# Kernel tuning notes

Measured on AMD Instinct MI355X. Metric: run time of the kernel, lower is better.

## Reference

```python
import jax, jax.numpy as jnp
import numpy as np
from jax import lax

silu = jax.nn.silu

def conv2d(x, w, b, pad):
    y = lax.conv_general_dilated(x, w, (1, 1), [(pad, pad), (pad, pad)],
                                 dimension_numbers=('NCHW', 'OIHW', 'NCHW'))
    return y + b[None, :, None, None]

def avgpool2(x):
    B, C, H, W = x.shape
    return x.reshape(B, C, H // 2, 2, W // 2, 2).mean(axis=(3, 5))

def up2x(x):
    # bilinear scale_factor=2, align_corners=True (matches F.interpolate)
    B, C, H, W = x.shape
    Ho, Wo = 2 * H, 2 * W
    ys = jnp.arange(Ho, dtype=x.dtype) * ((H - 1) / (Ho - 1))
    xs = jnp.arange(Wo, dtype=x.dtype) * ((W - 1) / (Wo - 1))
    y0 = jnp.floor(ys).astype(jnp.int32); y1 = jnp.minimum(y0 + 1, H - 1); wy = ys - y0
    x0 = jnp.floor(xs).astype(jnp.int32); x1 = jnp.minimum(x0 + 1, W - 1); wx = xs - x0
    row = x[:, :, y0, :] * (1 - wy)[None, None, :, None] + x[:, :, y1, :] * wy[None, None, :, None]
    return row[:, :, :, x0] * (1 - wx) + row[:, :, :, x1] * wx

def deform_conv2d(x, offset, weight, groups):
    # torchvision DeformConv2d semantics: stride=1, pad=(k-1)//2, dilation=1, no bias
    B, Cin, H, W = x.shape
    Cout, cpg, kh, kw = weight.shape  # cpg = Cin // groups
    K = kh * kw
    OG = offset.shape[1] // (2 * K)   # offset groups
    Cog = Cin // OG
    off = offset.reshape(B, OG, K, 2, H, W)  # (dy, dx) per kernel tap
    ki = jnp.repeat(jnp.arange(kh, dtype=x.dtype) - (kh - 1) // 2, kw)  # [K]
    kj = jnp.tile(jnp.arange(kw, dtype=x.dtype) - (kw - 1) // 2, kh)
    py = off[:, :, :, 0] + jnp.arange(H, dtype=x.dtype)[None, None, None, :, None] + ki[None, None, :, None, None]
    px = off[:, :, :, 1] + jnp.arange(W, dtype=x.dtype)[None, None, None, None, :] + kj[None, None, :, None, None]
    y0f = jnp.floor(py); x0f = jnp.floor(px)
    ly = py - y0f; lx = px - x0f
    y0 = y0f.astype(jnp.int32); x0 = x0f.astype(jnp.int32)
    xg = x.reshape(B, OG, Cog, H * W)

    def corner(yi, xi, wt):
        valid = (yi >= 0) & (yi < H) & (xi >= 0) & (xi < W)
        idx = jnp.clip(yi, 0, H - 1) * W + jnp.clip(xi, 0, W - 1)        # [B,OG,K,H,W]
        idxf = jnp.broadcast_to(idx.reshape(B, OG, 1, K * H * W), (B, OG, Cog, K * H * W))
        v = jnp.take_along_axis(xg, idxf, axis=3).reshape(B, OG, Cog, K, H, W)
        return v * (wt * valid)[:, :, None]

    val = (corner(y0, x0, (1 - ly) * (1 - lx)) + corner(y0, x0 + 1, (1 - ly) * lx)
           + corner(y0 + 1, x0, ly * (1 - lx)) + corner(y0 + 1, x0 + 1, ly * lx))
    # grouped contraction over sampled taps
    valg = val.reshape(B, groups, Cin // groups, K, H, W)
    wg = weight.reshape(groups, Cout // groups, cpg, K)
    return jnp.einsum('bgckhw,gock->bgohw', valg, wg).reshape(B, Cout, H, W)

def setup_inputs() -> dict:
    key = jax.random.key(0)
    ks = iter(jax.random.split(key, 64))
    def w(shape, s=0.05):
        return jax.random.normal(next(ks), shape, jnp.float32) * s
    B, H, W = 4, 512, 512
    d = {'x': jax.random.normal(next(ks), (B, 4, H, W), jnp.float32)}
    # offset estimators (small scale so sampled offsets stay moderate)
    d['eo1_w1'] = w((18, 4, 5, 5), 0.02);  d['eo1_b1'] = w((18,), 0.02)
    d['eo1_w2'] = w((36, 18, 5, 5), 0.02); d['eo1_b2'] = w((36,), 0.02)
    d['dcw1'] = w((2, 2, 3, 3))            # DeformConv2d(4->2, groups=2)
    d['c1d_w1'] = w((4, 2, 3, 3));   d['c1d_b1'] = w((4,))
    d['c1d_w2'] = w((8, 4, 3, 3));   d['c1d_b2'] = w((8,))
    d['eo2_w1'] = w((18, 8, 5, 5), 0.02);  d['eo2_b1'] = w((18,), 0.02)
    d['eo2_w2'] = w((36, 18, 5, 5), 0.02); d['eo2_b2'] = w((36,), 0.02)
    d['dcw2'] = w((8, 4, 3, 3))            # DeformConv2d(8->8, groups=2)
    d['c2d_w1'] = w((12, 8, 3, 3));  d['c2d_b1'] = w((12,))
    d['c2d_w2'] = w((16, 12, 3, 3)); d['c2d_b2'] = w((16,))
    d['eo3_w1'] = w((18, 16, 5, 5), 0.02); d['eo3_b1'] = w((18,), 0.02)
    d['eo3_w2'] = w((36, 18, 5, 5), 0.02); d['eo3_b2'] = w((36,), 0.02)
    d['dcw3'] = w((16, 8, 3, 3))           # DeformConv2d(16->16, groups=2)
    d['c3d_w1'] = w((14, 16, 3, 3)); d['c3d_b1'] = w((14,))
    d['c3d_w2'] = w((12, 14, 3, 3)); d['c3d_b2'] = w((12,))
    d['up2_w'] = w((12, 12, 3, 3));  d['up2_b'] = w((12,))
    d['c2u_w1'] = w((16, 28, 3, 3)); d['c2u_b1'] = w((16,))
    d['c2u_w2'] = w((8, 16, 3, 3));  d['c2u_b2'] = w((8,))
    d['up1_w'] = w((8, 8, 3, 3));    d['up1_b'] = w((8,))
    d['c1u_w1'] = w((8, 16, 3, 3));  d['c1u_b1'] = w((8,))
    d['c1u_w2'] = w((2, 8, 3, 3));   d['c1u_b2'] = w((2,))
    return d

def reference(x, eo1_w1, eo1_b1, eo1_w2, eo1_b2, dcw1, c1d_w1, c1d_b1, c1d_w2, c1d_b2,
              eo2_w1, eo2_b1, eo2_w2, eo2_b2, dcw2, c2d_w1, c2d_b1, c2d_w2, c2d_b2,
              eo3_w1, eo3_b1, eo3_w2, eo3_b2, dcw3, c3d_w1, c3d_b1, c3d_w2, c3d_b2,
              up2_w, up2_b, c2u_w1, c2u_b1, c2u_w2, c2u_b2, up1_w, up1_b,
              c1u_w1, c1u_b1, c1u_w2, c1u_b2):
    def convbasic(h, w1, b1, w2, b2):
        return silu(conv2d(silu(conv2d(h, w1, b1, 1)), w2, b2, 1))
    # level 1 down
    off1 = conv2d(conv2d(x, eo1_w1, eo1_b1, 2), eo1_w2, eo1_b2, 2)
    comp1 = deform_conv2d(x, off1, dcw1, groups=2)
    conv1_d = convbasic(comp1, c1d_w1, c1d_b1, c1d_w2, c1d_b2)
    pool1 = avgpool2(conv1_d)
    # level 2 down
    off2 = conv2d(conv2d(pool1, eo2_w1, eo2_b1, 2), eo2_w2, eo2_b2, 2)
    comp2 = deform_conv2d(pool1, off2, dcw2, groups=2)
    conv2_d = convbasic(comp2, c2d_w1, c2d_b1, c2d_w2, c2d_b2)
    pool2 = avgpool2(conv2_d)
    # level 3 (bottleneck)
    off3 = conv2d(conv2d(pool2, eo3_w1, eo3_b1, 2), eo3_w2, eo3_b2, 2)
    comp3 = deform_conv2d(pool2, off3, dcw3, groups=2)
    conv3_d = convbasic(comp3, c3d_w1, c3d_b1, c3d_w2, c3d_b2)
    # up path
    usmpl2 = silu(conv2d(up2x(conv3_d), up2_w, up2_b, 1))
    conv2_u = convbasic(jnp.concatenate([usmpl2, conv2_d], axis=1), c2u_w1, c2u_b1, c2u_w2, c2u_b2)
    usmpl1 = silu(conv2d(up2x(conv2_u), up1_w, up1_b, 1))
    conv1_u = convbasic(jnp.concatenate([usmpl1, conv1_d], axis=1), c1u_w1, c1u_b1, c1u_w2, c1u_b2)
    return conv1_u
```

## Files before the change

kernel.cpp:

```cpp
#include <hip/hip_runtime.h>
#include <math.h>

#define THREADS 256
typedef __attribute__((ext_vector_type(2))) float f32x2;
typedef __attribute__((ext_vector_type(4))) float f32x4;

__device__ __forceinline__ float silu_f(float v) {
    return v / (1.f + __expf(-v));
}

__device__ __forceinline__ void pk_fma_lo(f32x2& d, f32x2 a, f32x2 b) {
    asm("v_pk_fma_f32 %0, %1, %2, %0 op_sel:[0,0,0] op_sel_hi:[0,1,1]"
        : "+v"(d) : "v"(a), "v"(b));
}
__device__ __forceinline__ void pk_fma_hi(f32x2& d, f32x2 a, f32x2 b) {
    asm("v_pk_fma_f32 %0, %1, %2, %0 op_sel:[1,0,0] op_sel_hi:[1,1,1]"
        : "+v"(d) : "v"(a), "v"(b));
}
__device__ __forceinline__ void pk_fma_lo_s(f32x2& d, f32x2 a, f32x2 b) {
    asm("v_pk_fma_f32 %0, %1, %2, %0 op_sel:[0,0,0] op_sel_hi:[0,1,1]"
        : "+v"(d) : "v"(a), "s"(b));
}
__device__ __forceinline__ void pk_fma_hi_s(f32x2& d, f32x2 a, f32x2 b) {
    asm("v_pk_fma_f32 %0, %1, %2, %0 op_sel:[1,0,0] op_sel_hi:[1,1,1]"
        : "+v"(d) : "v"(a), "s"(b));
}

struct TEnt { const float* src; int dst; int cin; int cout; int k2; int base; int n; };
struct TTab { TEnt e[40]; int total; };

__global__ __launch_bounds__(THREADS)
void transpose_w_k(TTab t, float* __restrict__ tw) {
    const int i = blockIdx.x * THREADS + threadIdx.x;
    if (i >= t.total) return;
    int j = 0;
    while (i >= t.e[j].base + t.e[j].n) ++j;
    const TEnt e = t.e[j];
    const int local = i - e.base;
    const int co  = local % e.cout;
    const int tmp = local / e.cout;
    const int k   = tmp % e.k2;
    const int ci  = tmp / e.k2;
    tw[e.dst + local] = e.src[(co * e.cin + ci) * e.k2 + k];
}

template<int KS, int PX>
__device__ __forceinline__ void load_row(float* __restrict__ rr,
                                         const float* __restrict__ rp,
                                         bool vy, int x0, int W)
{
    constexpr int PAD = (KS - 1) / 2;
    constexpr int RW = PX + KS - 1;
#pragma unroll
    for (int q = -1; q <= PX / 4; ++q) {
        if (4 * q + 3 + PAD < 0 || 4 * q + PAD >= RW) continue;
        const int xs = x0 + 4 * q;
        const bool safe = (q >= 0) && (4 * q + 3 < PX);
        float vc[4] = {0.f, 0.f, 0.f, 0.f};
        if (safe) {
            if (vy) {
                const float4 v = *reinterpret_cast<const float4*>(rp + xs);
                vc[0] = v.x; vc[1] = v.y; vc[2] = v.z; vc[3] = v.w;
            }
        } else if (vy && xs >= 0 && xs + 4 <= W) {
            const float4 v = *reinterpret_cast<const float4*>(rp + xs);
            vc[0] = v.x; vc[1] = v.y; vc[2] = v.z; vc[3] = v.w;
        } else if (vy) {
#pragma unroll
            for (int c = 0; c < 4; ++c)
                vc[c] = ((unsigned)(xs + c) < (unsigned)W) ? rp[xs + c] : 0.f;
        }
#pragma unroll
        for (int c = 0; c < 4; ++c) {
            const int t = 4 * q + c + PAD;
            if (t >= 0 && t < RW) rr[t] = vc[c];
        }
    }
}

template<int CIN, int COUT, int KS, int PX, int PHASE, int RW2, int NP>
__device__ __forceinline__ void chan_body(
    const float* __restrict__ ip0, const float* __restrict__ wz,
    int cl, int y, int x0, int W, int H, int lw, int total,
    f32x2 (&r2)[2][RW2], f32x2 (&wb)[2][NP], f32x2 (&acc)[NP][PX])
{
    constexpr int PAD = (KS - 1) / 2;
    constexpr int K2 = KS * KS;
    static_assert(K2 % 2 == 1, "parity continuity needs odd K2");
#pragma unroll
    for (int ky = 0; ky < KS; ++ky) {
        {
            const bool last = (ky + 1 == KS);
            const int ncl = cl + (last ? 1 : 0);
            const int nky = last ? 0 : (ky + 1);
            if (!last || ncl < CIN) {
                const int yy = y + nky - PAD;
                load_row<KS, PX>((float*)r2[(PHASE + ky + 1) & 1],
                                 ip0 + (size_t)ncl * total + (yy << lw),
                                 (unsigned)yy < (unsigned)H, x0, W);
            }
        }
#pragma unroll
        for (int kx = 0; kx < KS; ++kx) {
            const int t = ky * KS + kx;
            const int wc = (PHASE + t) & 1;
            if (t + 1 < K2 || cl + 1 < CIN) {
                const f32x2* __restrict__ nx =
                    (const f32x2*)(wz + (size_t)(cl * K2 + t + 1) * COUT);
#pragma unroll
                for (int p = 0; p < NP; ++p) wb[wc ^ 1][p] = nx[p];
            }
#pragma unroll
            for (int p = 0; p < NP; ++p) {
                const f32x2 wp = wb[wc][p];
#pragma unroll
                for (int j = 0; j < PX; ++j) {
                    const int e = kx + j;
                    if (e & 1) pk_fma_hi_s(acc[p][j], r2[(PHASE + ky) & 1][e >> 1], wp);
                    else       pk_fma_lo_s(acc[p][j], r2[(PHASE + ky) & 1][e >> 1], wp);
                }
            }
            __builtin_amdgcn_sched_barrier(0);
        }
    }
}

template<int CIN, int COUT, int KS, bool ACT, int PX>
__global__ __launch_bounds__(THREADS)
void conv_sl_k(const float* __restrict__ in, const float* __restrict__ wt,
               const float* __restrict__ bias, float* __restrict__ out,
               int H, int lw, int bs_in, int bs_out, int nb, int nz)
{
    constexpr int PAD = (KS - 1) / 2;
    constexpr int K2 = KS * KS;
    constexpr int NP = COUT / 2;
    constexpr int RW = PX + KS - 1;
    constexpr int RW2 = (RW + 1) / 2;
    static_assert(CIN % 2 == 0 && COUT % 2 == 0 && PX % 4 == 0, "");

    const int lin = blockIdx.x;
    const int r8 = lin & 7;
    int q = lin >> 3;
    const int z = q % nz; q /= nz;
    const int g = q * 8 + r8;
    const int b = g % nb;
    const int xb = g / nb;

    const float* __restrict__ wz = wt + (size_t)z * (CIN * K2 * COUT);
    const int W = 1 << lw;
    const int total = H << lw;
    const int idx = (xb * THREADS + threadIdx.x) * PX;
    const float* ip0 = in + (size_t)b * bs_in;
    float* op = out + (size_t)b * bs_out + (size_t)z * COUT * total;
    const int x0 = idx & (W - 1);
    const int y  = idx >> lw;

    f32x2 acc[NP][PX];
#pragma unroll
    for (int p = 0; p < NP; ++p) {
        f32x2 bb;
        bb.x = bias[z * COUT + 2 * p];
        bb.y = bias[z * COUT + 2 * p + 1];
#pragma unroll
        for (int j = 0; j < PX; ++j) acc[p][j] = bb;
    }

    f32x2 r2[2][RW2];
    f32x2 wb[2][NP];
    {
        const int yy = y - PAD;
        load_row<KS, PX>((float*)r2[0], ip0 + (yy << lw),
                         (unsigned)yy < (unsigned)H, x0, W);
        const f32x2* __restrict__ w0 = (const f32x2*)wz;
#pragma unroll
        for (int p = 0; p < NP; ++p) wb[0][p] = w0[p];
    }

#pragma unroll 1
    for (int c2 = 0; c2 < CIN / 2; ++c2) {
        chan_body<CIN, COUT, KS, PX, 0, RW2, NP>(ip0, wz, 2 * c2,     y, x0, W, H, lw, total, r2, wb, acc);
        chan_body<CIN, COUT, KS, PX, 1, RW2, NP>(ip0, wz, 2 * c2 + 1, y, x0, W, H, lw, total, r2, wb, acc);
    }

#pragma unroll
    for (int p = 0; p < NP; ++p) {
#pragma unroll
        for (int h = 0; h < 2; ++h) {
            const int co = 2 * p + h;
#pragma unroll
            for (int j4 = 0; j4 < PX / 4; ++j4) {
                float4 v;
                float a0 = h ? acc[p][4 * j4 + 0].y : acc[p][4 * j4 + 0].x;
                float a1 = h ? acc[p][4 * j4 + 1].y : acc[p][4 * j4 + 1].x;
                float a2 = h ? acc[p][4 * j4 + 2].y : acc[p][4 * j4 + 2].x;
                float a3 = h ? acc[p][4 * j4 + 3].y : acc[p][4 * j4 + 3].x;
                v.x = ACT ? silu_f(a0) : a0;
                v.y = ACT ? silu_f(a1) : a1;
                v.z = ACT ? silu_f(a2) : a2;
                v.w = ACT ? silu_f(a3) : a3;
                *reinterpret_cast<float4*>(op + (size_t)co * total + idx + 4 * j4) = v;
            }
        }
    }
}

template<int CIN, int COUT, int KS, bool ACT, int PX>
__global__ __launch_bounds__(THREADS)
void conv_k(const float* __restrict__ in, const float* __restrict__ wt,
            const float* __restrict__ bias, float* __restrict__ out,
            int H, int lw, int bs_in, int bs_out)
{
    constexpr int PAD = (KS - 1) / 2;
    constexpr int K2 = KS * KS;
    constexpr int CO_S = (COUT + 3) & ~3;
    constexpr int WQ = CO_S / 4;
    constexpr int NP = COUT / 2;
    constexpr int RW = PX + KS - 1;
    constexpr int RW2 = (RW + 1) / 2;
    static_assert(COUT % 2 == 0, "");
    __shared__ float sw[CIN * K2 * CO_S];

    const int W = 1 << lw;
    const int total = H << lw;
    const int idx = (blockIdx.x * THREADS + threadIdx.x) * PX;
    const float* ip0 = in + (size_t)blockIdx.y * bs_in;
    float* op = out + (size_t)blockIdx.y * bs_out;
    const int x0 = idx & (W - 1);
    const int y  = idx >> lw;

    for (int i = threadIdx.x; i < CIN * K2 * COUT; i += THREADS)
        sw[(i / COUT) * CO_S + i % COUT] = wt[i];
    __syncthreads();

    f32x2 acc[NP][PX];
#pragma unroll
    for (int p = 0; p < NP; ++p) {
        f32x2 bb;
        bb.x = bias[2 * p];
        bb.y = bias[2 * p + 1];
#pragma unroll
        for (int j = 0; j < PX; ++j) acc[p][j] = bb;
    }

#pragma unroll 1
    for (int cl = 0; cl < CIN; ++cl) {
        const float* __restrict__ row0 = ip0 + (size_t)cl * total;
        f32x2 r2[KS][RW2];
#pragma unroll
        for (int ky = 0; ky < KS; ++ky) {
            const int yy = y + ky - PAD;
            load_row<KS, PX>((float*)r2[ky], row0 + (yy << lw),
                             (unsigned)yy < (unsigned)H, x0, W);
        }
        const float* __restrict__ wbase = &sw[cl * K2 * CO_S];
#pragma unroll
        for (int t = 0; t < K2; ++t) {
            const int ky = t / KS, kx = t % KS;
            const f32x4* __restrict__ wv = (const f32x4*)(wbase + t * CO_S);
#pragma unroll
            for (int q = 0; q < WQ; ++q) {
                const f32x4 w4 = wv[q];
                const f32x2 wlo = __builtin_shufflevector(w4, w4, 0, 1);
                const f32x2 whi = __builtin_shufflevector(w4, w4, 2, 3);
#pragma unroll
                for (int s = 0; s < 2; ++s) {
                    const int p = 2 * q + s;
                    if (p < NP) {
                        const f32x2 wp = s ? whi : wlo;
#pragma unroll
                        for (int j = 0; j < PX; ++j) {
                            const int e = kx + j;
                            if (e & 1) pk_fma_hi(acc[p][j], r2[ky][e >> 1], wp);
                            else       pk_fma_lo(acc[p][j], r2[ky][e >> 1], wp);
                        }
                    }
                }
            }
            __builtin_amdgcn_sched_barrier(0);
        }
    }

#pragma unroll
    for (int p = 0; p < NP; ++p) {
#pragma unroll
        for (int h = 0; h < 2; ++h) {
            const int co = 2 * p + h;
            if (PX == 2) {
                float2 v;
                float a0 = h ? acc[p][0].y : acc[p][0].x;
                float a1 = h ? acc[p][1].y : acc[p][1].x;
                v.x = ACT ? silu_f(a0) : a0;
                v.y = ACT ? silu_f(a1) : a1;
                *reinterpret_cast<float2*>(op + (size_t)co * total + idx) = v;
            } else {
#pragma unroll
                for (int j4 = 0; j4 < PX / 4; ++j4) {
                    float4 v;
                    float a0 = h ? acc[p][4 * j4 + 0].y : acc[p][4 * j4 + 0].x;
                    float a1 = h ? acc[p][4 * j4 + 1].y : acc[p][4 * j4 + 1].x;
                    float a2 = h ? acc[p][4 * j4 + 2].y : acc[p][4 * j4 + 2].x;
                    float a3 = h ? acc[p][4 * j4 + 3].y : acc[p][4 * j4 + 3].x;
                    v.x = ACT ? silu_f(a0) : a0;
                    v.y = ACT ? silu_f(a1) : a1;
                    v.z = ACT ? silu_f(a2) : a2;
                    v.w = ACT ? silu_f(a3) : a3;
                    *reinterpret_cast<float4*>(op + (size_t)co * total + idx + 4 * j4) = v;
                }
            }
        }
    }
}

template<int CIN, int COUT>
__global__ __launch_bounds__(THREADS)
void dconv_k(const float* __restrict__ in, const float* __restrict__ off,
             const float* __restrict__ twg0, const float* __restrict__ twg1,
             float* __restrict__ out,
             int H, int lw, int bs_in, int bs_off, int bs_out)
{
    constexpr int K = 9;
    constexpr int OG = 2;
    constexpr int COG = CIN / OG;
    constexpr int COUTG = COUT / 2;
    constexpr int NWG = COG * K * COUTG;
    __shared__ float sw[2 * NWG];
    for (int i = threadIdx.x; i < 2 * NWG; i += THREADS)
        sw[i] = (i < NWG) ? twg0[i] : twg1[i - NWG];
    __syncthreads();

    const int W = 1 << lw;
    const int total = H << lw;
    const int idx = blockIdx.x * THREADS + threadIdx.x;
    const float* ip0 = in + (size_t)blockIdx.y * bs_in;
    const float* offp = off + (size_t)blockIdx.y * bs_off;
    float* op = out + (size_t)blockIdx.y * bs_out;
    const int x = idx & (W - 1);
    const int y = idx >> lw;

    float acc[COUT];
#pragma unroll
    for (int co = 0; co < COUT; ++co) acc[co] = 0.f;

#pragma unroll
    for (int og = 0; og < OG; ++og) {
#pragma unroll
        for (int k = 0; k < K; ++k) {
            const int ki = k / 3 - 1;
            const int kj = k % 3 - 1;
            const float dy = offp[(size_t)(((og * K + k) * 2 + 0)) * total + idx];
            const float dx = offp[(size_t)(((og * K + k) * 2 + 1)) * total + idx];
            const float py = dy + (float)(y + ki);
            const float px = dx + (float)(x + kj);
            const float y0f = floorf(py), x0f = floorf(px);
            const float ly = py - y0f, lx = px - x0f;
            const int y0 = (int)y0f, x0 = (int)x0f;
            const int y1 = y0 + 1, x1 = x0 + 1;
            const bool vy0 = (unsigned)y0 < (unsigned)H;
            const bool vy1 = (unsigned)y1 < (unsigned)H;
            const bool vx0 = (unsigned)x0 < (unsigned)W;
            const bool vx1 = (unsigned)x1 < (unsigned)W;
            const int cy0 = min(max(y0, 0), H - 1), cy1 = min(max(y1, 0), H - 1);
            const int cx0 = min(max(x0, 0), W - 1), cx1 = min(max(x1, 0), W - 1);
            const int i00 = (cy0 << lw) + cx0, i01 = (cy0 << lw) + cx1;
            const int i10 = (cy1 << lw) + cx0, i11 = (cy1 << lw) + cx1;
            const float f00 = (vy0 && vx0) ? (1.f - ly) * (1.f - lx) : 0.f;
            const float f01 = (vy0 && vx1) ? (1.f - ly) * lx : 0.f;
            const float f10 = (vy1 && vx0) ? ly * (1.f - lx) : 0.f;
            const float f11 = (vy1 && vx1) ? ly * lx : 0.f;
            const float* swg = &sw[og * NWG];
#pragma unroll
            for (int c = 0; c < COG; ++c) {
                const float* __restrict__ ip = ip0 + (size_t)(og * COG + c) * total;
                const float v = f00 * ip[i00] + f01 * ip[i01]
                              + f10 * ip[i10] + f11 * ip[i11];
                const float* __restrict__ wr = &swg[(c * K + k) * COUTG];
#pragma unroll
                for (int col = 0; col < COUTG; ++col)
                    acc[og * COUTG + col] = fmaf(v, wr[col], acc[og * COUTG + col]);
            }
        }
    }

#pragma unroll
    for (int co = 0; co < COUT; ++co)
        op[(size_t)co * total + idx] = acc[co];
}

__global__ __launch_bounds__(THREADS)
void avgpool_k(const float* __restrict__ in, float* __restrict__ out,
               int n, int lt, int lwo, int bsi, int bso)
{
    const int idx = blockIdx.x * THREADS + threadIdx.x;
    if (idx >= n) return;
    const float* ip0 = in + (size_t)blockIdx.y * bsi;
    float* op = out + (size_t)blockIdx.y * bso;
    const int c = idx >> lt;
    const int r = idx & ((1 << lt) - 1);
    const int oy = r >> lwo;
    const int ox = r & ((1 << lwo) - 1);
    const int Wi = 2 << lwo;
    const float* ip = ip0 + ((size_t)c << (lt + 2)) + ((size_t)(2 * oy) << (lwo + 1)) + 2 * ox;
    const float2 t = *reinterpret_cast<const float2*>(ip);
    const float2 b = *reinterpret_cast<const float2*>(ip + Wi);
    op[idx] = 0.25f * (t.x + t.y + b.x + b.y);
}

__global__ __launch_bounds__(THREADS)
void up2x_k(const float* __restrict__ in, float* __restrict__ out,
            int n, int lt, int lwo, int Hin, int bsi, int bso)
{
    const int idx = blockIdx.x * THREADS + threadIdx.x;
    if (idx >= n) return;
    const float* ip0 = in + (size_t)blockIdx.y * bsi;
    float* op = out + (size_t)blockIdx.y * bso;
    const int c = idx >> lt;
    const int r = idx & ((1 << lt) - 1);
    const int oy = r >> lwo;
    const int ox = r & ((1 << lwo) - 1);
    const int W = 1 << (lwo - 1);
    const int H = Hin;
    const float s = (float)(H - 1) / (float)(2 * H - 1);
    const float fy = (float)oy * s;
    const float fx = (float)ox * s;
    const int y0 = (int)fy;
    const int x0 = (int)fx;
    const int y1 = min(y0 + 1, H - 1);
    const int x1 = min(x0 + 1, W - 1);
    const float wy = fy - (float)y0;
    const float wx = fx - (float)x0;
    const float* ip = ip0 + ((size_t)c << (lt - 2));
    const float v00 = ip[y0 * W + x0], v01 = ip[y0 * W + x1];
    const float v10 = ip[y1 * W + x0], v11 = ip[y1 * W + x1];
    op[idx] = (v00 * (1.f - wy) + v10 * wy) * (1.f - wx)
            + (v01 * (1.f - wy) + v11 * wy) * wx;
}

__global__ __launch_bounds__(THREADS)
void copy_k(float4* __restrict__ dst, const float4* __restrict__ src,
            int n4, int bsd, int bss)
{
    const int i = blockIdx.x * THREADS + threadIdx.x;
    if (i >= n4) return;
    dst[(size_t)blockIdx.y * bsd + i] = src[(size_t)blockIdx.y * bss + i];
}


extern "C" void kernel_launch(void* const* d_in, const int* in_sizes, int n_in,
                              void* d_out, int out_size, void* d_ws, size_t ws_size,
                              hipStream_t stream) {
    const float* x      = (const float*)d_in[0];
    const float* eo1_b1 = (const float*)d_in[2];
    const float* eo1_b2 = (const float*)d_in[4];
    const float* c1d_b1 = (const float*)d_in[7];
    const float* c1d_b2 = (const float*)d_in[9];
    const float* eo2_b1 = (const float*)d_in[11];
    const float* eo2_b2 = (const float*)d_in[13];
    const float* c2d_b1 = (const float*)d_in[16];
    const float* c2d_b2 = (const float*)d_in[18];
    const float* eo3_b1 = (const float*)d_in[20];
    const float* eo3_b2 = (const float*)d_in[22];
    const float* c3d_b1 = (const float*)d_in[25];
    const float* c3d_b2 = (const float*)d_in[27];
    const float* up2_b  = (const float*)d_in[29];
    const float* c2u_b1 = (const float*)d_in[31];
    const float* c2u_b2 = (const float*)d_in[33];
    const float* up1_b  = (const float*)d_in[35];
    const float* c1u_b1 = (const float*)d_in[37];
    const float* c1u_b2 = (const float*)d_in[39];

    float* out = (float*)d_out;
    float* wsf = (float*)d_ws;

    constexpr int H1 = 512, A1 = H1 * H1;
    constexpr int H2 = 256, A2 = H2 * H2;
    constexpr int H3 = 128, A3 = H3 * H3;
    constexpr int TW_FLOATS = 81920;
    constexpr int SLOT = 58 * A1;

    const int widx[34]  = {1, 1, 1,  3, 3, 3, 3, 3,  6, 8,
                           10, 10, 10,  12, 12, 12, 12, 12,  15, 17,
                           19,  21, 21, 21, 21, 21,  24, 26,
                           28, 30, 32, 34, 36, 38};
    const int wcin[34]  = {4, 4, 4,  18, 18, 18, 18, 18,  2, 4,
                           8, 8, 8,  18, 18, 18, 18, 18,  8, 12,
                           16,  18, 18, 18, 18, 18,  16, 14,
                           12, 28, 16, 8, 16, 8};
    const int wcout[34] = {6, 6, 6,  8, 8, 8, 8, 4,  4, 8,
                           6, 6, 6,  8, 8, 8, 8, 4,  12, 16,
                           18,  8, 8, 8, 8, 4,  14, 12,
                           12, 16, 8, 8, 8, 2};
    const int wk2[34]   = {25, 25, 25,  25, 25, 25, 25, 25,  9, 9,
                           25, 25, 25,  25, 25, 25, 25, 25,  9, 9,
                           25,  25, 25, 25, 25, 25,  9, 9,
                           9, 9, 9, 9, 9, 9};
    const int wsoff[34] = {0, 600, 1200,  0, 3600, 7200, 10800, 14400,  0, 0,
                           0, 1200, 2400,  0, 3600, 7200, 10800, 14400,  0, 0,
                           0,  0, 3600, 7200, 10800, 14400,  0, 0,
                           0, 0, 0, 0, 0, 0};
    const int cont[34]  = {1, 1, 0,  1, 1, 1, 0, 0,  0, 0,
                           1, 1, 0,  1, 1, 1, 0, 0,  0, 0,
                           0,  1, 1, 1, 0, 0,  0, 0,
                           0, 0, 0, 0, 0, 0};
    TTab tab;
    const float* tw[40];
    int off = 0, base = 0;
    for (int i = 0; i < 34; ++i) {
        const int n = wcin[i] * wcout[i] * wk2[i];
        tab.e[i].src = (const float*)d_in[widx[i]] + wsoff[i];
        tab.e[i].dst = off; tab.e[i].cin = wcin[i]; tab.e[i].cout = wcout[i];
        tab.e[i].k2 = wk2[i]; tab.e[i].base = base; tab.e[i].n = n;
        tw[i] = wsf + off;
        off = cont[i] ? (off + n) : ((off + n + 63) & ~63);
        base += n;
    }
    const int didx[3]   = {5, 14, 23};
    const int dcoutg[3] = {1, 4, 8};
    const int dcpg[3]   = {2, 4, 8};
    for (int i = 0; i < 3; ++i) {
        for (int g = 0; g < 2; ++g) {
            const int e = 34 + 2 * i + g;
            const int n = dcoutg[i] * dcpg[i] * 9;
            tab.e[e].src = (const float*)d_in[didx[i]] + (size_t)g * n;
            tab.e[e].dst = off; tab.e[e].cin = dcpg[i]; tab.e[e].cout = dcoutg[i];
            tab.e[e].k2 = 9; tab.e[e].base = base; tab.e[e].n = n;
            tw[e] = wsf + off;
            off = (off + n + 63) & ~63;
            base += n;
        }
    }
    tab.total = base;
    transpose_w_k<<<(base + THREADS - 1) / THREADS, THREADS, 0, stream>>>(tab, wsf);

    int B = 4;
    while (B > 1 && ws_size < ((size_t)TW_FLOATS + (size_t)B * SLOT) * sizeof(float)) B >>= 1;

    auto run_all = [&](int Bc, float* slot, int SB,
                       const float* xin, int xbs, float* outp, int obs) {
        float* S0 = slot;
        float* S1 = S0 + 36 * A1;
        float* S2 = S1 + 18 * A1;
        float* P  = S2 + 2 * A1;
        float* L1 = S1 + 10 * A1;
        float* L2 = S0 + 32 * A1;
        auto gs = [&](int n, int px, int z) { return dim3((n / (px * THREADS)) * Bc * z); };
        auto gp = [&](int n, int px) { return dim3(n / (px * THREADS), Bc); };
        auto g1 = [&](int n) { return dim3((n + THREADS - 1) / THREADS, Bc); };

        conv_sl_k<4, 6, 5, false, 8><<<gs(A1, 8, 3), THREADS, 0, stream>>>(xin, tw[0], eo1_b1, S1, H1, 9, xbs, SB, Bc, 3);
        conv_sl_k<18, 8, 5, false, 8><<<gs(A1, 8, 4), THREADS, 0, stream>>>(S1, tw[3], eo1_b2, S0, H1, 9, SB, SB, Bc, 4);
        conv_sl_k<18, 4, 5, false, 8><<<gs(A1, 8, 1), THREADS, 0, stream>>>(S1, tw[7], eo1_b2 + 32, S0 + 32 * A1, H1, 9, SB, SB, Bc, 1);
        dconv_k<4, 2><<<g1(A1), THREADS, 0, stream>>>(xin, S0, tw[34], tw[35], S2, H1, 9, xbs, SB, SB);
        conv_k<2, 4, 3, true, 8><<<gp(A1, 8), THREADS, 0, stream>>>(S2, tw[8], c1d_b1, S1, H1, 9, SB, SB);
        conv_k<4, 8, 3, true, 8><<<gp(A1, 8), THREADS, 0, stream>>>(S1, tw[9], c1d_b2, L1, H1, 9, SB, SB);
        avgpool_k<<<g1(8 * A2), THREADS, 0, stream>>>(L1, P, 8 * A2, 16, 8, SB, SB);

        conv_sl_k<8, 6, 5, false, 8><<<gs(A2, 8, 3), THREADS, 0, stream>>>(P, tw[10], eo2_b1, S1, H2, 8, SB, SB, Bc, 3);
        conv_sl_k<18, 8, 5, false, 8><<<gs(A2, 8, 4), THREADS, 0, stream>>>(S1, tw[13], eo2_b2, S0, H2, 8, SB, SB, Bc, 4);
        conv_sl_k<18, 4, 5, false, 8><<<gs(A2, 8, 1), THREADS, 0, stream>>>(S1, tw[17], eo2_b2 + 32, S0 + 32 * A2, H2, 8, SB, SB, Bc, 1);
        dconv_k<8, 8><<<g1(A2), THREADS, 0, stream>>>(P, S0, tw[36], tw[37], S2, H2, 8, SB, SB, SB);
        conv_k<8, 12, 3, true, 4><<<gp(A2, 4), THREADS, 0, stream>>>(S2, tw[18], c2d_b1, S1, H2, 8, SB, SB);
        conv_k<12, 16, 3, true, 4><<<gp(A2, 4), THREADS, 0, stream>>>(S1, tw[19], c2d_b2, L2, H2, 8, SB, SB);
        avgpool_k<<<g1(16 * A3), THREADS, 0, stream>>>(L2, P, 16 * A3, 14, 7, SB, SB);

        conv_k<16, 18, 5, false, 2><<<gp(A3, 2), THREADS, 0, stream>>>(P, tw[20], eo3_b1, S1, H3, 7, SB, SB);
        conv_sl_k<18, 8, 5, false, 4><<<gs(A3, 4, 4), THREADS, 0, stream>>>(S1, tw[21], eo3_b2, S0, H3, 7, SB, SB, Bc, 4);
        conv_sl_k<18, 4, 5, false, 4><<<gs(A3, 4, 1), THREADS, 0, stream>>>(S1, tw[25], eo3_b2 + 32, S0 + 32 * A3, H3, 7, SB, SB, Bc, 1);
        dconv_k<16, 16><<<g1(A3), THREADS, 0, stream>>>(P, S0, tw[38], tw[39], S2, H3, 7, SB, SB, SB);
        conv_k<16, 14, 3, true, 2><<<gp(A3, 2), THREADS, 0, stream>>>(S2, tw[26], c3d_b1, S1, H3, 7, SB, SB);
        conv_k<14, 12, 3, true, 2><<<gp(A3, 2), THREADS, 0, stream>>>(S1, tw[27], c3d_b2, S2, H3, 7, SB, SB);

        up2x_k<<<g1(12 * A2), THREADS, 0, stream>>>(S2, S0, 12 * A2, 16, 8, H3, SB, SB);
        conv_k<12, 12, 3, true, 4><<<gp(A2, 4), THREADS, 0, stream>>>(S0, tw[28], up2_b, S1, H2, 8, SB, SB);
        copy_k<<<g1(4 * A2), THREADS, 0, stream>>>((float4*)(S1 + 12 * A2), (const float4*)L2,
                                                   4 * A2, SB / 4, SB / 4);
        conv_k<28, 16, 3, true, 4><<<gp(A2, 4), THREADS, 0, stream>>>(S1, tw[29], c2u_b1, S0, H2, 8, SB, SB);
        conv_k<16, 8, 3, true, 4><<<gp(A2, 4), THREADS, 0, stream>>>(S0, tw[30], c2u_b2, S2, H2, 8, SB, SB);

        up2x_k<<<g1(8 * A1), THREADS, 0, stream>>>(S2, S0, 8 * A1, 18, 9, H2, SB, SB);
        conv_k<8, 8, 3, true, 8><<<gp(A1, 8), THREADS, 0, stream>>>(S0, tw[31], up1_b, S0 + 8 * A1, H1, 9, SB, SB);
        copy_k<<<g1(2 * A1), THREADS, 0, stream>>>((float4*)(S0 + 16 * A1), (const float4*)L1,
                                                   2 * A1, SB / 4, SB / 4);
        conv_k<16, 8, 3, true, 8><<<gp(A1, 8), THREADS, 0, stream>>>(S0 + 8 * A1, tw[32], c1u_b1, S1, H1, 9, SB, SB);
        conv_k<8, 2, 3, true, 8><<<gp(A1, 8), THREADS, 0, stream>>>(S1, tw[33], c1u_b2, outp, H1, 9, SB, obs);
    };

    for (int g = 0; g < 4; g += B)
        run_all(B, wsf + TW_FLOATS, SLOT,
                x + (size_t)g * 4 * A1, 4 * A1,
                out + (size_t)g * 2 * A1, 2 * A1);
}
```

Measured before the change: 1.541 ms.

## Read skip connections directly in conv and widen offset convs to fewer launches

Adds a two-input convolution kernel that reads the upsampled branch and the skip tensor from separate buffers, which removes the concatenation copy kernels. The second offset convolution at each level now uses a 12-output-channel slice kernel in 3 slices, replacing one 8-channel launch with 4 slices plus a separate 4-channel launch. The weight transform table is rebuilt to match. Together these cut launches and memory traffic, at the cost of more registers per thread in the wider offset conv.

```diff
diff --git a/kernel.cpp b/kernel.cpp
--- a/kernel.cpp
+++ b/kernel.cpp
@@ -204,82 +204,43 @@
     }
 }
 
-template<int CIN, int COUT, int KS, bool ACT, int PX>
-__global__ __launch_bounds__(THREADS)
-void conv_k(const float* __restrict__ in, const float* __restrict__ wt,
-            const float* __restrict__ bias, float* __restrict__ out,
-            int H, int lw, int bs_in, int bs_out)
-{
-    constexpr int PAD = (KS - 1) / 2;
+template<int COUT, int KS, int PX, int WQ, int NP, int RW2>
+__device__ __forceinline__ void lds_taps(
+    const float* __restrict__ wbase, f32x2 (&r2)[KS][RW2], f32x2 (&acc)[NP][PX])
+{
     constexpr int K2 = KS * KS;
     constexpr int CO_S = (COUT + 3) & ~3;
-    constexpr int WQ = CO_S / 4;
-    constexpr int NP = COUT / 2;
-    constexpr int RW = PX + KS - 1;
-    constexpr int RW2 = (RW + 1) / 2;
-    static_assert(COUT % 2 == 0, "");
-    __shared__ float sw[CIN * K2 * CO_S];
-
-    const int W = 1 << lw;
-    const int total = H << lw;
-    const int idx = (blockIdx.x * THREADS + threadIdx.x) * PX;
-    const float* ip0 = in + (size_t)blockIdx.y * bs_in;
-    float* op = out + (size_t)blockIdx.y * bs_out;
-    const int x0 = idx & (W - 1);
-    const int y  = idx >> lw;
-
-    for (int i = threadIdx.x; i < CIN * K2 * COUT; i += THREADS)
-        sw[(i / COUT) * CO_S + i % COUT] = wt[i];
-    __syncthreads();
-
-    f32x2 acc[NP][PX];
-#pragma unroll
-    for (int p = 0; p < NP; ++p) {
-        f32x2 bb;
-        bb.x = bias[2 * p];
-        bb.y = bias[2 * p + 1];
-#pragma unroll
-        for (int j = 0; j < PX; ++j) acc[p][j] = bb;
-    }
-
-#pragma unroll 1
-    for (int cl = 0; cl < CIN; ++cl) {
-        const float* __restrict__ row0 = ip0 + (size_t)cl * total;
-        f32x2 r2[KS][RW2];
-#pragma unroll
-        for (int ky = 0; ky < KS; ++ky) {
-            const int yy = y + ky - PAD;
-            load_row<KS, PX>((float*)r2[ky], row0 + (yy << lw),
-                             (unsigned)yy < (unsigned)H, x0, W);
-        }
-        const float* __restrict__ wbase = &sw[cl * K2 * CO_S];
-#pragma unroll
-        for (int t = 0; t < K2; ++t) {
-            const int ky = t / KS, kx = t % KS;
-            const f32x4* __restrict__ wv = (const f32x4*)(wbase + t * CO_S);
-#pragma unroll
-            for (int q = 0; q < WQ; ++q) {
-                const f32x4 w4 = wv[q];
-                const f32x2 wlo = __builtin_shufflevector(w4, w4, 0, 1);
-                const f32x2 whi = __builtin_shufflevector(w4, w4, 2, 3);
-#pragma unroll
-                for (int s = 0; s < 2; ++s) {
-                    const int p = 2 * q + s;
-                    if (p < NP) {
-                        const f32x2 wp = s ? whi : wlo;
-#pragma unroll
-                        for (int j = 0; j < PX; ++j) {
-                            const int e = kx + j;
-                            if (e & 1) pk_fma_hi(acc[p][j], r2[ky][e >> 1], wp);
-                            else       pk_fma_lo(acc[p][j], r2[ky][e >> 1], wp);
-                        }
+#pragma unroll
+    for (int t = 0; t < K2; ++t) {
+        const int ky = t / KS, kx = t % KS;
+        const f32x4* __restrict__ wv = (const f32x4*)(wbase + t * CO_S);
+#pragma unroll
+        for (int q = 0; q < WQ; ++q) {
+            const f32x4 w4 = wv[q];
+            const f32x2 wlo = __builtin_shufflevector(w4, w4, 0, 1);
+            const f32x2 whi = __builtin_shufflevector(w4, w4, 2, 3);
+#pragma unroll
+            for (int s = 0; s < 2; ++s) {
+                const int p = 2 * q + s;
+                if (p < NP) {
+                    const f32x2 wp = s ? whi : wlo;
+#pragma unroll
+                    for (int j = 0; j < PX; ++j) {
+                        const int e = kx + j;
+                        if (e & 1) pk_fma_hi(acc[p][j], r2[ky][e >> 1], wp);
+                        else       pk_fma_lo(acc[p][j], r2[ky][e >> 1], wp);
                     }
                 }
             }
-            __builtin_amdgcn_sched_barrier(0);
-        }
-    }
-
+        }
+        __builtin_amdgcn_sched_barrier(0);
+    }
+}
+
+template<int COUT, int PX, bool ACT, int NP>
+__device__ __forceinline__ void conv_store(
+    float* __restrict__ op, int total, int idx, f32x2 (&acc)[NP][PX])
+{
 #pragma unroll
     for (int p = 0; p < NP; ++p) {
 #pragma unroll
@@ -309,6 +270,118 @@
             }
         }
     }
+}
+
+template<int CIN, int COUT, int KS, bool ACT, int PX>
+__global__ __launch_bounds__(THREADS)
+void conv_k(const float* __restrict__ in, const float* __restrict__ wt,
+            const float* __restrict__ bias, float* __restrict__ out,
+            int H, int lw, int bs_in, int bs_out)
+{
+    constexpr int PAD = (KS - 1) / 2;
+    constexpr int K2 = KS * KS;
+    constexpr int CO_S = (COUT + 3) & ~3;
+    constexpr int WQ = CO_S / 4;
+    constexpr int NP = COUT / 2;
+    constexpr int RW = PX + KS - 1;
+    constexpr int RW2 = (RW + 1) / 2;
+    static_assert(COUT % 2 == 0, "");
+    __shared__ float sw[CIN * K2 * CO_S];
+
+    const int W = 1 << lw;
+    const int total = H << lw;
+    const int idx = (blockIdx.x * THREADS + threadIdx.x) * PX;
+    const float* ip0 = in + (size_t)blockIdx.y * bs_in;
+    float* op = out + (size_t)blockIdx.y * bs_out;
+    const int x0 = idx & (W - 1);
+    const int y  = idx >> lw;
+
+    for (int i = threadIdx.x; i < CIN * K2 * COUT; i += THREADS)
+        sw[(i / COUT) * CO_S + i % COUT] = wt[i];
+    __syncthreads();
+
+    f32x2 acc[NP][PX];
+#pragma unroll
+    for (int p = 0; p < NP; ++p) {
+        f32x2 bb;
+        bb.x = bias[2 * p];
+        bb.y = bias[2 * p + 1];
+#pragma unroll
+        for (int j = 0; j < PX; ++j) acc[p][j] = bb;
+    }
+
+#pragma unroll 1
+    for (int cl = 0; cl < CIN; ++cl) {
+        const float* __restrict__ row0 = ip0 + (size_t)cl * total;
+        f32x2 r2[KS][RW2];
+#pragma unroll
+        for (int ky = 0; ky < KS; ++ky) {
+            const int yy = y + ky - PAD;
+            load_row<KS, PX>((float*)r2[ky], row0 + (yy << lw),
+                             (unsigned)yy < (unsigned)H, x0, W);
+        }
+        lds_taps<COUT, KS, PX, WQ, NP, RW2>(&sw[cl * K2 * CO_S], r2, acc);
+    }
+
+    conv_store<COUT, PX, ACT, NP>(op, total, idx, acc);
+}
+
+template<int C1, int C2, int COUT, int KS, bool ACT, int PX>
+__global__ __launch_bounds__(THREADS)
+void conv2in_k(const float* __restrict__ in0, const float* __restrict__ in1,
+               const float* __restrict__ wt, const float* __restrict__ bias,
+               float* __restrict__ out, int H, int lw,
+               int bs_in0, int bs_in1, int bs_out)
+{
+    constexpr int CIN = C1 + C2;
+    constexpr int PAD = (KS - 1) / 2;
+    constexpr int K2 = KS * KS;
+    constexpr int CO_S = (COUT + 3) & ~3;
+    constexpr int WQ = CO_S / 4;
+    constexpr int NP = COUT / 2;
+    constexpr int RW = PX + KS - 1;
+    constexpr int RW2 = (RW + 1) / 2;
+    static_assert(COUT % 2 == 0, "");
+    __shared__ float sw[CIN * K2 * CO_S];
+
+    const int W = 1 << lw;
+    const int total = H << lw;
+    const int idx = (blockIdx.x * THREADS + threadIdx.x) * PX;
+    const float* ip0 = in0 + (size_t)blockIdx.y * bs_in0;
+    const float* ip1 = in1 + (size_t)blockIdx.y * bs_in1;
+    float* op = out + (size_t)blockIdx.y * bs_out;
+    const int x0 = idx & (W - 1);
+    const int y  = idx >> lw;
+
+    for (int i = threadIdx.x; i < CIN * K2 * COUT; i += THREADS)
+        sw[(i / COUT) * CO_S + i % COUT] = wt[i];
+    __syncthreads();
+
+    f32x2 acc[NP][PX];
+#pragma unroll
+    for (int p = 0; p < NP; ++p) {
+        f32x2 bb;
+        bb.x = bias[2 * p];
+        bb.y = bias[2 * p + 1];
+#pragma unroll
+        for (int j = 0; j < PX; ++j) acc[p][j] = bb;
+    }
+
+#pragma unroll 1
+    for (int cl = 0; cl < CIN; ++cl) {
+        const float* __restrict__ row0 =
+            (cl < C1) ? (ip0 + (size_t)cl * total) : (ip1 + (size_t)(cl - C1) * total);
+        f32x2 r2[KS][RW2];
+#pragma unroll
+        for (int ky = 0; ky < KS; ++ky) {
+            const int yy = y + ky - PAD;
+            load_row<KS, PX>((float*)r2[ky], row0 + (yy << lw),
+                             (unsigned)yy < (unsigned)H, x0, W);
+        }
+        lds_taps<COUT, KS, PX, WQ, NP, RW2>(&sw[cl * K2 * CO_S], r2, acc);
+    }
+
+    conv_store<COUT, PX, ACT, NP>(op, total, idx, acc);
 }
 
 template<int CIN, int COUT>
@@ -435,15 +508,6 @@
             + (v01 * (1.f - wy) + v11 * wy) * wx;
 }
 
-__global__ __launch_bounds__(THREADS)
-void copy_k(float4* __restrict__ dst, const float4* __restrict__ src,
-            int n4, int bsd, int bss)
-{
-    const int i = blockIdx.x * THREADS + threadIdx.x;
-    if (i >= n4) return;
-    dst[(size_t)blockIdx.y * bsd + i] = src[(size_t)blockIdx.y * bss + i];
-}
-
 
 extern "C" void kernel_launch(void* const* d_in, const int* in_sizes, int n_in,
                               void* d_out, int out_size, void* d_ws, size_t ws_size,
@@ -476,35 +540,36 @@
     constexpr int H3 = 128, A3 = H3 * H3;
     constexpr int TW_FLOATS = 81920;
     constexpr int SLOT = 58 * A1;
-
-    const int widx[34]  = {1, 1, 1,  3, 3, 3, 3, 3,  6, 8,
-                           10, 10, 10,  12, 12, 12, 12, 12,  15, 17,
-                           19,  21, 21, 21, 21, 21,  24, 26,
-                           28, 30, 32, 34, 36, 38};
-    const int wcin[34]  = {4, 4, 4,  18, 18, 18, 18, 18,  2, 4,
-                           8, 8, 8,  18, 18, 18, 18, 18,  8, 12,
-                           16,  18, 18, 18, 18, 18,  16, 14,
-                           12, 28, 16, 8, 16, 8};
-    const int wcout[34] = {6, 6, 6,  8, 8, 8, 8, 4,  4, 8,
-                           6, 6, 6,  8, 8, 8, 8, 4,  12, 16,
-                           18,  8, 8, 8, 8, 4,  14, 12,
-                           12, 16, 8, 8, 8, 2};
-    const int wk2[34]   = {25, 25, 25,  25, 25, 25, 25, 25,  9, 9,
-                           25, 25, 25,  25, 25, 25, 25, 25,  9, 9,
-                           25,  25, 25, 25, 25, 25,  9, 9,
-                           9, 9, 9, 9, 9, 9};
-    const int wsoff[34] = {0, 600, 1200,  0, 3600, 7200, 10800, 14400,  0, 0,
-                           0, 1200, 2400,  0, 3600, 7200, 10800, 14400,  0, 0,
-                           0,  0, 3600, 7200, 10800, 14400,  0, 0,
-                           0, 0, 0, 0, 0, 0};
-    const int cont[34]  = {1, 1, 0,  1, 1, 1, 0, 0,  0, 0,
-                           1, 1, 0,  1, 1, 1, 0, 0,  0, 0,
-                           0,  1, 1, 1, 0, 0,  0, 0,
-                           0, 0, 0, 0, 0, 0};
+    constexpr int NCONV = 28;
+
+    const int widx[NCONV]  = {1, 1, 1,  3, 3, 3,  6, 8,
+                              10, 10, 10,  12, 12, 12,  15, 17,
+                              19,  21, 21, 21,  24, 26,
+                              28, 30, 32, 34, 36, 38};
+    const int wcin[NCONV]  = {4, 4, 4,  18, 18, 18,  2, 4,
+                              8, 8, 8,  18, 18, 18,  8, 12,
+                              16,  18, 18, 18,  16, 14,
+                              12, 28, 16, 8, 16, 8};
+    const int wcout[NCONV] = {6, 6, 6,  12, 12, 12,  4, 8,
+                              6, 6, 6,  12, 12, 12,  12, 16,
+                              18,  12, 12, 12,  14, 12,
+                              12, 16, 8, 8, 8, 2};
+    const int wk2[NCONV]   = {25, 25, 25,  25, 25, 25,  9, 9,
+                              25, 25, 25,  25, 25, 25,  9, 9,
+                              25,  25, 25, 25,  9, 9,
+                              9, 9, 9, 9, 9, 9};
+    const int wsoff[NCONV] = {0, 600, 1200,  0, 5400, 10800,  0, 0,
+                              0, 1200, 2400,  0, 5400, 10800,  0, 0,
+                              0,  0, 5400, 10800,  0, 0,
+                              0, 0, 0, 0, 0, 0};
+    const int cont[NCONV]  = {1, 1, 0,  1, 1, 0,  0, 0,
+                              1, 1, 0,  1, 1, 0,  0, 0,
+                              0,  1, 1, 0,  0, 0,
+                              0, 0, 0, 0, 0, 0};
     TTab tab;
     const float* tw[40];
     int off = 0, base = 0;
-    for (int i = 0; i < 34; ++i) {
+    for (int i = 0; i < NCONV; ++i) {
         const int n = wcin[i] * wcout[i] * wk2[i];
         tab.e[i].src = (const float*)d_in[widx[i]] + wsoff[i];
         tab.e[i].dst = off; tab.e[i].cin = wcin[i]; tab.e[i].cout = wcout[i];
@@ -518,7 +583,7 @@
     const int dcpg[3]   = {2, 4, 8};
     for (int i = 0; i < 3; ++i) {
         for (int g = 0; g < 2; ++g) {
-            const int e = 34 + 2 * i + g;
+            const int e = NCONV + 2 * i + g;
             const int n = dcoutg[i] * dcpg[i] * 9;
             tab.e[e].src = (const float*)d_in[didx[i]] + (size_t)g * n;
             tab.e[e].dst = off; tab.e[e].cin = dcpg[i]; tab.e[e].cout = dcoutg[i];
@@ -547,41 +612,34 @@
         auto g1 = [&](int n) { return dim3((n + THREADS - 1) / THREADS, Bc); };
 
         conv_sl_k<4, 6, 5, false, 8><<<gs(A1, 8, 3), THREADS, 0, stream>>>(xin, tw[0], eo1_b1, S1, H1, 9, xbs, SB, Bc, 3);
-        conv_sl_k<18, 8, 5, false, 8><<<gs(A1, 8, 4), THREADS, 0, stream>>>(S1, tw[3], eo1_b2, S0, H1, 9, SB, SB, Bc, 4);
-        conv_sl_k<18, 4, 5, false, 8><<<gs(A1, 8, 1), THREADS, 0, stream>>>(S1, tw[7], eo1_b2 + 32, S0 + 32 * A1, H1, 9, SB, SB, Bc, 1);
-        dconv_k<4, 2><<<g1(A1), THREADS, 0, stream>>>(xin, S0, tw[34], tw[35], S2, H1, 9, xbs, SB, SB);
-        conv_k<2, 4, 3, true, 8><<<gp(A1, 8), THREADS, 0, stream>>>(S2, tw[8], c1d_b1, S1, H1, 9, SB, SB);
-        conv_k<4, 8, 3, true, 8><<<gp(A1, 8), THREADS, 0, stream>>>(S1, tw[9], c1d_b2, L1, H1, 9, SB, SB);
+        conv_sl_k<18, 12, 5, false, 8><<<gs(A1, 8, 3), THREADS, 0, stream>>>(S1, tw[3], eo1_b2, S0, H1, 9, SB, SB, Bc, 3);
+        dconv_k<4, 2><<<g1(A1), THREADS, 0, stream>>>(xin, S0, tw[28], tw[29], S2, H1, 9, xbs, SB, SB);
+        conv_k<2, 4, 3, true, 8><<<gp(A1, 8), THREADS, 0, stream>>>(S2, tw[6], c1d_b1, S1, H1, 9, SB, SB);
+        conv_k<4, 8, 3, true, 8><<<gp(A1, 8), THREADS, 0, stream>>>(S1, tw[7], c1d_b2, L1, H1, 9, SB, SB);
         avgpool_k<<<g1(8 * A2), THREADS, 0, stream>>>(L1, P, 8 * A2, 16, 8, SB, SB);
 
-        conv_sl_k<8, 6, 5, false, 8><<<gs(A2, 8, 3), THREADS, 0, stream>>>(P, tw[10], eo2_b1, S1, H2, 8, SB, SB, Bc, 3);
-        conv_sl_k<18, 8, 5, false, 8><<<gs(A2, 8, 4), THREADS, 0, stream>>>(S1, tw[13], eo2_b2, S0, H2, 8, SB, SB, Bc, 4);
-        conv_sl_k<18, 4, 5, false, 8><<<gs(A2, 8, 1), THREADS, 0, stream>>>(S1, tw[17], eo2_b2 + 32, S0 + 32 * A2, H2, 8, SB, SB, Bc, 1);
-        dconv_k<8, 8><<<g1(A2), THREADS, 0, stream>>>(P, S0, tw[36], tw[37], S2, H2, 8, SB, SB, SB);
-        conv_k<8, 12, 3, true, 4><<<gp(A2, 4), THREADS, 0, stream>>>(S2, tw[18], c2d_b1, S1, H2, 8, SB, SB);
-        conv_k<12, 16, 3, true, 4><<<gp(A2, 4), THREADS, 0, stream>>>(S1, tw[19], c2d_b2, L2, H2, 8, SB, SB);
+        conv_sl_k<8, 6, 5, false, 8><<<gs(A2, 8, 3), THREADS, 0, stream>>>(P, tw[8], eo2_b1, S1, H2, 8, SB, SB, Bc, 3);
+        conv_sl_k<18, 12, 5, false, 8><<<gs(A2, 8, 3), THREADS, 0, stream>>>(S1, tw[11], eo2_b2, S0, H2, 8, SB, SB, Bc, 3);
+        dconv_k<8, 8><<<g1(A2), THREADS, 0, stream>>>(P, S0, tw[30], tw[31], S2, H2, 8, SB, SB, SB);
+        conv_k<8, 12, 3, true, 4><<<gp(A2, 4), THREADS, 0, stream>>>(S2, tw[14], c2d_b1, S1, H2, 8, SB, SB);
+        conv_k<12, 16, 3, true, 4><<<gp(A2, 4), THREADS, 0, stream>>>(S1, tw[15], c2d_b2, L2, H2, 8, SB, SB);
         avgpool_k<<<g1(16 * A3), THREADS, 0, stream>>>(L2, P, 16 * A3, 14, 7, SB, SB);
 
-        conv_k<16, 18, 5, false, 2><<<gp(A3, 2), THREADS, 0, stream>>>(P, tw[20], eo3_b1, S1, H3, 7, SB, SB);
-        conv_sl_k<18, 8, 5, false, 4><<<gs(A3, 4, 4), THREADS, 0, stream>>>(S1, tw[21], eo3_b2, S0, H3, 7, SB, SB, Bc, 4);
-        conv_sl_k<18, 4, 5, false, 4><<<gs(A3, 4, 1), THREADS, 0, stream>>>(S1, tw[25], eo3_b2 + 32, S0 + 32 * A3, H3, 7, SB, SB, Bc, 1);
-        dconv_k<16, 16><<<g1(A3), THREADS, 0, stream>>>(P, S0, tw[38], tw[39], S2, H3, 7, SB, SB, SB);
-        conv_k<16, 14, 3, true, 2><<<gp(A3, 2), THREADS, 0, stream>>>(S2, tw[26], c3d_b1, S1, H3, 7, SB, SB);
-        conv_k<14, 12, 3, true, 2><<<gp(A3, 2), THREADS, 0, stream>>>(S1, tw[27], c3d_b2, S2, H3, 7, SB, SB);
+        conv_k<16, 18, 5, false, 2><<<gp(A3, 2), THREADS, 0, stream>>>(P, tw[16], eo3_b1, S1, H3, 7, SB, SB);
+        conv_sl_k<18, 12, 5, false, 4><<<gs(A3, 4, 3), THREADS, 0, stream>>>(S1, tw[17], eo3_b2, S0, H3, 7, SB, SB, Bc, 3);
+        dconv_k<16, 16><<<g1(A3), THREADS, 0, stream>>>(P, S0, tw[32], tw[33], S2, H3, 7, SB, SB, SB);
+        conv_k<16, 14, 3, true, 2><<<gp(A3, 2), THREADS, 0, stream>>>(S2, tw[20], c3d_b1, S1, H3, 7, SB, SB);
+        conv_k<14, 12, 3, true, 2><<<gp(A3, 2), THREADS, 0, stream>>>(S1, tw[21], c3d_b2, S2, H3, 7, SB, SB);
 
         up2x_k<<<g1(12 * A2), THREADS, 0, stream>>>(S2, S0, 12 * A2, 16, 8, H3, SB, SB);
-        conv_k<12, 12, 3, true, 4><<<gp(A2, 4), THREADS, 0, stream>>>(S0, tw[28], up2_b, S1, H2, 8, SB, SB);
-        copy_k<<<g1(4 * A2), THREADS, 0, stream>>>((float4*)(S1 + 12 * A2), (const float4*)L2,
-                                                   4 * A2, SB / 4, SB / 4);
-        conv_k<28, 16, 3, true, 4><<<gp(A2, 4), THREADS, 0, stream>>>(S1, tw[29], c2u_b1, S0, H2, 8, SB, SB);
-        conv_k<16, 8, 3, true, 4><<<gp(A2, 4), THREADS, 0, stream>>>(S0, tw[30], c2u_b2, S2, H2, 8, SB, SB);
+        conv_k<12, 12, 3, true, 4><<<gp(A2, 4), THREADS, 0, stream>>>(S0, tw[22], up2_b, S1, H2, 8, SB, SB);
+        conv2in_k<12, 16, 16, 3, true, 4><<<gp(A2, 4), THREADS, 0, stream>>>(S1, L2, tw[23], c2u_b1, S0, H2, 8, SB, SB, SB);
+        conv_k<16, 8, 3, true, 4><<<gp(A2, 4), THREADS, 0, stream>>>(S0, tw[24], c2u_b2, S2, H2, 8, SB, SB);
 
         up2x_k<<<g1(8 * A1), THREADS, 0, stream>>>(S2, S0, 8 * A1, 18, 9, H2, SB, SB);
-        conv_k<8, 8, 3, true, 8><<<gp(A1, 8), THREADS, 0, stream>>>(S0, tw[31], up1_b, S0 + 8 * A1, H1, 9, SB, SB);
-        copy_k<<<g1(2 * A1), THREADS, 0, stream>>>((float4*)(S0 + 16 * A1), (const float4*)L1,
-                                                   2 * A1, SB / 4, SB / 4);
-        conv_k<16, 8, 3, true, 8><<<gp(A1, 8), THREADS, 0, stream>>>(S0 + 8 * A1, tw[32], c1u_b1, S1, H1, 9, SB, SB);
-        conv_k<8, 2, 3, true, 8><<<gp(A1, 8), THREADS, 0, stream>>>(S1, tw[33], c1u_b2, outp, H1, 9, SB, obs);
+        conv_k<8, 8, 3, true, 8><<<gp(A1, 8), THREADS, 0, stream>>>(S0, tw[25], up1_b, S0 + 8 * A1, H1, 9, SB, SB);
+        conv2in_k<8, 8, 8, 3, true, 8><<<gp(A1, 8), THREADS, 0, stream>>>(S0 + 8 * A1, L1, tw[26], c1u_b1, S1, H1, 9, SB, SB, SB);
+        conv_k<8, 2, 3, true, 8><<<gp(A1, 8), THREADS, 0, stream>>>(S1, tw[27], c1u_b2, outp, H1, 9, SB, obs);
     };
 
     for (int g = 0; g < 4; g += B)
```

After: 1.404 ms. -8.9%, faster.
